# Performance work log

Hardware: AMD Instinct MI355X
Metric: run time of the kernel (lower is better)

The kernel has to match this reference:

```python
import jax, jax.numpy as jnp
import numpy as np

B, L, D = 16, 512, 768   # batch, seq_len, hidden_size
H = 12                   # encoder attention heads (self_attention_scores)
K = 128                  # num_preserved_tokens
U, NH = 256, 4           # router attention num_units / num_heads


def setup_inputs() -> dict:
    key = jax.random.key(0)
    ks = jax.random.split(key, 8)
    hidden_states = jax.random.normal(ks[0], (B, L, D), dtype=jnp.float32)
    u = jax.random.uniform(ks[1], (B, 1, 1, L))
    attention_mask = jnp.where(u < 0.9, 0.0, -10000.0).astype(jnp.float32)
    self_attention_scores = jax.random.normal(ks[2], (B, H, L, L), dtype=jnp.float32)
    Wq = jax.random.normal(ks[3], (U, D), dtype=jnp.float32) * 0.02
    Wk = jax.random.normal(ks[4], (U, D), dtype=jnp.float32) * 0.02
    Wv = jax.random.normal(ks[5], (U, D), dtype=jnp.float32) * 0.02
    Wo = jax.random.normal(ks[6], (D, U), dtype=jnp.float32) * 0.02
    bo = jnp.zeros((D,), dtype=jnp.float32)
    return {"hidden_states": hidden_states, "attention_mask": attention_mask,
            "self_attention_scores": self_attention_scores,
            "Wq": Wq, "Wk": Wk, "Wv": Wv, "Wo": Wo, "bo": bo}


def reference(hidden_states, attention_mask, self_attention_scores, Wq, Wk, Wv, Wo, bo):
    # sentence summary: softmax over additive mask -> weighted token average
    att = jax.nn.softmax(attention_mask, axis=-1)            # [B,1,1,L]
    sentences = jnp.einsum('bql,bld->bqd', att[:, 0], hidden_states)  # [B,1,D]

    key_padding_mask = attention_mask[:, 0, 0, :] < -10.0    # [B,L] True = masked

    # MyMultiHeadAttention(query=sentences, key=value=hidden_states)
    hd = U // NH
    q = jnp.einsum('bqd,ud->bqu', sentences, Wq)             # [B,1,U]
    k = jnp.einsum('bld,ud->blu', hidden_states, Wk)         # [B,L,U]
    v = jnp.einsum('bld,ud->blu', hidden_states, Wv)         # [B,L,U]
    qh = q.reshape(B, 1, NH, hd).transpose(2, 0, 1, 3)       # [h,B,1,hd]
    kh = k.reshape(B, L, NH, hd).transpose(2, 0, 1, 3)       # [h,B,L,hd]
    vh = v.reshape(B, L, NH, hd).transpose(2, 0, 1, 3)       # [h,B,L,hd]
    # NOTE: original scales by key_dim**0.5 = hidden_size**0.5 (not head dim)
    scores = jnp.einsum('hbqd,hbkd->hbqk', qh, kh) / (D ** 0.5)  # [h,B,1,L]
    scores = jnp.where(key_padding_mask[None, :, None, :], -jnp.inf, scores)
    probs = jax.nn.softmax(scores, axis=-1)
    out_h = jnp.einsum('hbqk,hbkd->hbqd', probs, vh)         # [h,B,1,hd]
    out = out_h.transpose(1, 2, 0, 3).reshape(B, 1, U)       # concat heads
    new_token = jnp.einsum('bqu,du->bqd', out, Wo) + bo      # [B,1,D]

    class_token = hidden_states[:, :1, :]                    # [B,1,D]

    # importance: mean over heads, sum over query positions -> [B,L]
    importance = self_attention_scores.mean(axis=1).sum(axis=1)
    top_idx = jax.lax.top_k(importance, K)[1]                # [B,K]
    # boolean-mask gather preserves original token order -> sort indices
    sorted_idx = jnp.sort(top_idx, axis=-1)                  # [B,K]
    preserved_tokens = jnp.take_along_axis(hidden_states, sorted_idx[:, :, None], axis=1)  # [B,K,D]
    preserved_mask = jnp.take_along_axis(attention_mask[:, 0, 0, :], sorted_idx, axis=1)
    preserved_mask = preserved_mask.reshape(B, 1, 1, K)

    zmask = jnp.zeros((B, 1, 1, 1), dtype=attention_mask.dtype)
    final_token = jnp.concatenate([class_token, preserved_tokens, new_token], axis=1)  # [B,K+2,D]
    final_attention_mask = jnp.concatenate([zmask, preserved_mask, zmask], axis=-1)    # [B,1,1,K+2]
    return final_token, final_attention_mask
```

## Files before the change

### kernel.cpp

```cpp
#include <hip/hip_runtime.h>
#include <math.h>

#define B_ 16
#define L_ 512
#define D_ 768
#define H_ 12
#define K_ 128
#define U_ 256
#define NH_ 4
#define HD_ 64
#define OUTROWS_ 130
#define IMPCH_ 64

__global__ __launch_bounds__(768) void front_kernel(
    const float* __restrict__ sas, const float* __restrict__ hidden,
    const float* __restrict__ mask, float* __restrict__ part,
    float* __restrict__ sent_part) {
  const int t = threadIdx.x;
  if (blockIdx.x < B_ * IMPCH_) {
    __shared__ float4 lbuf[6][128];
    const int b = blockIdx.x >> 6, chunk = blockIdx.x & 63;
    const int col4 = t & 127;
    const int rg = t >> 7;
    const float4* base = (const float4*)sas +
        ((size_t)(b * (H_ * L_) + chunk * 96 + rg * 16)) * 128 + col4;
    float4 a = make_float4(0.f, 0.f, 0.f, 0.f);
    #pragma unroll
    for (int k = 0; k < 16; ++k) {
      float4 v = base[(size_t)k * 128];
      a.x += v.x; a.y += v.y; a.z += v.z; a.w += v.w;
    }
    lbuf[rg][col4] = a;
    __syncthreads();
    if (rg == 0) {
      float4 o = lbuf[0][col4];
      #pragma unroll
      for (int g = 1; g < 6; ++g) {
        float4 v = lbuf[g][col4];
        o.x += v.x; o.y += v.y; o.z += v.z; o.w += v.w;
      }
      const float s = 1.0f / 12.0f;
      o.x *= s; o.y *= s; o.z *= s; o.w *= s;
      ((float4*)part)[((size_t)b * IMPCH_ + chunk) * 128 + col4] = o;
    }
  } else {
    __shared__ float att[L_];
    __shared__ float red_m[12], red_s[12];
    __shared__ float4 cbuf[4][192];
    const int i = blockIdx.x - B_ * IMPCH_;
    const int b = i >> 4, chunk = i & 15;
    const int wave = t >> 6, lane = t & 63;
    const float m = (t < L_) ? mask[b * L_ + t] : -INFINITY;
    float r = m;
    #pragma unroll
    for (int off = 32; off > 0; off >>= 1) r = fmaxf(r, __shfl_down(r, off, 64));
    if (lane == 0) red_m[wave] = r;
    __syncthreads();
    float mx = red_m[0];
    #pragma unroll
    for (int w = 1; w < 12; ++w) mx = fmaxf(mx, red_m[w]);
    const float e = (t < L_) ? expf(m - mx) : 0.f;
    float rs = e;
    #pragma unroll
    for (int off = 32; off > 0; off >>= 1) rs += __shfl_down(rs, off, 64);
    if (lane == 0) red_s[wave] = rs;
    __syncthreads();
    float se = 0.f;
    #pragma unroll
    for (int w = 0; w < 12; ++w) se += red_s[w];
    if (t < L_) att[t] = e / se;
    __syncthreads();
    const int c4 = t % 192, sub = t / 192;
    const int l0 = chunk * 32 + sub * 8;
    const float4* h4 = (const float4*)hidden + ((size_t)b * L_ + l0) * 192 + c4;
    float4 acc = make_float4(0.f, 0.f, 0.f, 0.f);
    #pragma unroll
    for (int ii = 0; ii < 8; ++ii) {
      const float w = att[l0 + ii];
      const float4 hv = h4[(size_t)ii * 192];
      acc.x += w * hv.x; acc.y += w * hv.y; acc.z += w * hv.z; acc.w += w * hv.w;
    }
    cbuf[sub][c4] = acc;
    __syncthreads();
    if (t < 192) {
      float4 o = cbuf[0][t];
      #pragma unroll
      for (int g = 1; g < 4; ++g) {
        const float4 v = cbuf[g][t];
        o.x += v.x; o.y += v.y; o.z += v.z; o.w += v.w;
      }
      ((float4*)sent_part)[((size_t)b * 16 + chunk) * 192 + t] = o;
    }
  }
}

__global__ __launch_bounds__(768) void qproj_topk_kernel(
    const float* __restrict__ sent_part, const float* __restrict__ Wq,
    const float* __restrict__ Wk, float* __restrict__ wqe,
    const float* __restrict__ part, const float* __restrict__ mask,
    const float* __restrict__ hidden, float* __restrict__ out0,
    float* __restrict__ out1, float* __restrict__ outv) {
  __shared__ float s[D_];
  __shared__ float qvh[HD_];
  __shared__ float v[L_];
  __shared__ int lidx[K_];
  __shared__ int wcnt[12];
  const int t = threadIdx.x;
  const int wave = t >> 6, lane = t & 63;

  if (blockIdx.x < 64) {
    const int b = blockIdx.x >> 2, h = blockIdx.x & 3;
    {
      const float* sp = sent_part + (size_t)b * 16 * D_ + t;
      float a = 0.f;
      #pragma unroll
      for (int c = 0; c < 16; ++c) a += sp[(size_t)c * D_];
      s[t] = a;
    }
    __syncthreads();
    for (int u = wave; u < HD_; u += 12) {
      const float* wr = Wq + (size_t)(h * HD_ + u) * D_;
      float acc = 0.f;
      #pragma unroll
      for (int k = 0; k < 12; ++k) {
        const int d = lane + (k << 6);
        acc += wr[d] * s[d];
      }
      #pragma unroll
      for (int o = 32; o > 0; o >>= 1) acc += __shfl_down(acc, o, 64);
      if (lane == 0) qvh[u] = acc;
    }
    __syncthreads();
    {
      float acc = 0.f;
      const float* wk = Wk + (size_t)(h * HD_) * D_ + t;
      #pragma unroll 4
      for (int j = 0; j < HD_; ++j) acc += qvh[j] * wk[(size_t)j * D_];
      wqe[((size_t)b * NH_ + h) * D_ + t] = acc;
    }
  } else {
    const int b = blockIdx.x - 64;
    if (t < U_) outv[b * U_ + t] = 0.f;
    if (t < L_) {
      const float* pp = part + (size_t)b * IMPCH_ * L_ + t;
      float sum = 0.f;
      #pragma unroll 8
      for (int g = 0; g < IMPCH_; ++g) sum += pp[(size_t)g * L_];
      v[t] = sum;
    }
    __syncthreads();
    bool sel = false;
    if (t < L_) {
      const float mv = v[t];
      int cnt = 0;
      #pragma unroll 8
      for (int j = 0; j < L_; ++j) {
        float o = v[j];
        cnt += (o > mv) || (o == mv && j < t);
      }
      sel = cnt < K_;
    }
    const unsigned long long ball = __ballot(sel);
    if (lane == 0) wcnt[wave] = __popcll(ball);
    __syncthreads();
    int base = 0;
    for (int w = 0; w < wave; ++w) base += wcnt[w];
    const int pos = base + __popcll(ball & ((1ull << lane) - 1ull));
    if (sel) {
      lidx[pos] = t;
      out1[b * OUTROWS_ + 1 + pos] = mask[b * L_ + t];
    }
    if (t == 0) {
      out1[b * OUTROWS_ + 0] = 0.f;
      out1[b * OUTROWS_ + OUTROWS_ - 1] = 0.f;
    }
    __syncthreads();
    const float4* hb4 = (const float4*)(hidden + (size_t)b * L_ * D_);
    float4* ob4 = (float4*)(out0 + (size_t)b * OUTROWS_ * D_);
    const int NG = (K_ + 1) * 192;
    for (int i = t; i < NG; i += 768) {
      const int r = i / 192;
      const int c = i - r * 192;
      const int src = (r == 0) ? 0 : lidx[r - 1];
      ob4[r * 192 + c] = hb4[src * 192 + c];
    }
  }
}

__global__ __launch_bounds__(256) void score_kernel(
    const float* __restrict__ hidden, const float* __restrict__ mask,
    const float* __restrict__ wqe, float* __restrict__ scores) {
  __shared__ float4 wq4[NH_ * 192];
  const int b = blockIdx.x, chunk = blockIdx.y, t = threadIdx.x;
  {
    const float4* wsrc = (const float4*)(wqe + (size_t)b * NH_ * D_);
    for (int i = t; i < NH_ * 192; i += 256) wq4[i] = wsrc[i];
  }
  __syncthreads();
  const int wave = t >> 6, lane = t & 63;
  const float scale = 0.03608439182435161f;
  #pragma unroll
  for (int r = 0; r < 8; ++r) {
    const int l = chunk * 32 + wave * 8 + r;
    const float4* hr4 = (const float4*)(hidden + ((size_t)b * L_ + l) * D_);
    float s0 = 0.f, s1 = 0.f, s2 = 0.f, s3 = 0.f;
    #pragma unroll
    for (int jj = 0; jj < 3; ++jj) {
      const int c = lane + 64 * jj;
      const float4 hv = hr4[c];
      const float4 w0 = wq4[0 * 192 + c];
      const float4 w1 = wq4[1 * 192 + c];
      const float4 w2 = wq4[2 * 192 + c];
      const float4 w3 = wq4[3 * 192 + c];
      s0 += hv.x * w0.x + hv.y * w0.y + hv.z * w0.z + hv.w * w0.w;
      s1 += hv.x * w1.x + hv.y * w1.y + hv.z * w1.z + hv.w * w1.w;
      s2 += hv.x * w2.x + hv.y * w2.y + hv.z * w2.z + hv.w * w2.w;
      s3 += hv.x * w3.x + hv.y * w3.y + hv.z * w3.z + hv.w * w3.w;
    }
    #pragma unroll
    for (int o = 32; o > 0; o >>= 1) {
      s0 += __shfl_down(s0, o, 64);
      s1 += __shfl_down(s1, o, 64);
      s2 += __shfl_down(s2, o, 64);
      s3 += __shfl_down(s3, o, 64);
    }
    if (lane == 0) {
      const bool kp = mask[b * L_ + l] < -10.f;
      float* sp = scores + (size_t)b * NH_ * L_ + l;
      sp[0 * L_] = kp ? -INFINITY : s0 * scale;
      sp[1 * L_] = kp ? -INFINITY : s1 * scale;
      sp[2 * L_] = kp ? -INFINITY : s2 * scale;
      sp[3 * L_] = kp ? -INFINITY : s3 * scale;
    }
  }
}

__global__ __launch_bounds__(768) void ctx_outv_kernel(
    const float* __restrict__ hidden, const float* __restrict__ scores,
    const float* __restrict__ Wv, float* __restrict__ outv) {
  __shared__ float pr[NH_][32];
  __shared__ float red_m[NH_][12], red_s[NH_][12];
  __shared__ __align__(16) float ctxs[NH_ * D_];
  const int b = blockIdx.x, chunk = blockIdx.y, t = threadIdx.x;
  const int wave = t >> 6, lane = t & 63;
  const int l0 = chunk * 32;

  float val[NH_];
  #pragma unroll
  for (int h = 0; h < NH_; ++h)
    val[h] = (t < L_) ? scores[((size_t)b * NH_ + h) * L_ + t] : -INFINITY;
  #pragma unroll
  for (int h = 0; h < NH_; ++h) {
    float r = val[h];
    #pragma unroll
    for (int off = 32; off > 0; off >>= 1) r = fmaxf(r, __shfl_down(r, off, 64));
    if (lane == 0) red_m[h][wave] = r;
  }
  __syncthreads();
  float e[NH_];
  #pragma unroll
  for (int h = 0; h < NH_; ++h) {
    float mx = red_m[h][0];
    #pragma unroll
    for (int w = 1; w < 12; ++w) mx = fmaxf(mx, red_m[h][w]);
    e[h] = (t < L_) ? expf(val[h] - mx) : 0.f;
    float rs = e[h];
    #pragma unroll
    for (int off = 32; off > 0; off >>= 1) rs += __shfl_down(rs, off, 64);
    if (lane == 0) red_s[h][wave] = rs;
  }
  __syncthreads();
  if (t >= l0 && t < l0 + 32) {
    #pragma unroll
    for (int h = 0; h < NH_; ++h) {
      float se = 0.f;
      #pragma unroll
      for (int w = 0; w < 12; ++w) se += red_s[h][w];
      pr[h][t - l0] = e[h] / se;
    }
  }
  __syncthreads();

  const int c4 = t % 192, hh = t / 192;
  const float4* h4 = (const float4*)hidden + ((size_t)b * L_ + l0) * 192 + c4;
  float4 acc = make_float4(0.f, 0.f, 0.f, 0.f);
  #pragma unroll 8
  for (int l = 0; l < 32; ++l) {
    const float w = pr[hh][l];
    const float4 hv = h4[(size_t)l * 192];
    acc.x += w * hv.x; acc.y += w * hv.y; acc.z += w * hv.z; acc.w += w * hv.w;
  }
  ((float4*)ctxs)[hh * 192 + c4] = acc;
  __syncthreads();

  for (int hu = wave; hu < U_; hu += 12) {
    const float* wr = Wv + (size_t)hu * D_;
    const float* ch = ctxs + (hu >> 6) * D_;
    float a = 0.f;
    #pragma unroll
    for (int k = 0; k < 12; ++k) {
      const int d = lane + (k << 6);
      a += wr[d] * ch[d];
    }
    #pragma unroll
    for (int off = 32; off > 0; off >>= 1) a += __shfl_down(a, off, 64);
    if (lane == 0) atomicAdd(&outv[b * U_ + hu], a);
  }
}

__global__ __launch_bounds__(192) void newtoken_kernel(
    const float* __restrict__ outv, const float* __restrict__ Wo,
    const float* __restrict__ bo, float* __restrict__ out0) {
  __shared__ float4 ov4[64];
  const int b = blockIdx.x, q = blockIdx.y, t = threadIdx.x;
  const int wave = t >> 6, lane = t & 63;
  if (t < 64) ov4[t] = ((const float4*)(outv + b * U_))[t];
  __syncthreads();
  const int dbase = q * 192 + wave * 64;
  const float4 o = ov4[lane];
  for (int i = 0; i < 64; ++i) {
    const int d = dbase + i;
    const float4 w = ((const float4*)(Wo + (size_t)d * U_))[lane];
    float acc = w.x * o.x + w.y * o.y + w.z * o.z + w.w * o.w;
    #pragma unroll
    for (int off = 32; off > 0; off >>= 1) acc += __shfl_down(acc, off, 64);
    if (lane == 0)
      out0[((size_t)b * OUTROWS_ + (OUTROWS_ - 1)) * D_ + d] = bo[d] + acc;
  }
}

extern "C" void kernel_launch(void* const* d_in, const int* in_sizes, int n_in,
                              void* d_out, int out_size, void* d_ws, size_t ws_size,
                              hipStream_t stream) {
  const float* hidden = (const float*)d_in[0];
  const float* mask   = (const float*)d_in[1];
  const float* sas    = (const float*)d_in[2];
  const float* Wq     = (const float*)d_in[3];
  const float* Wk     = (const float*)d_in[4];
  const float* Wv     = (const float*)d_in[5];
  const float* Wo     = (const float*)d_in[6];
  const float* bo     = (const float*)d_in[7];

  float* out0 = (float*)d_out;
  float* out1 = out0 + (size_t)B_ * OUTROWS_ * D_;

  float* part      = (float*)d_ws;
  float* sent_part = part + (size_t)B_ * IMPCH_ * L_;
  float* wqe       = sent_part + (size_t)B_ * 16 * D_;
  float* scores    = wqe + (size_t)B_ * NH_ * D_;
  float* outv      = scores + (size_t)B_ * NH_ * L_;

  front_kernel<<<B_ * IMPCH_ + B_ * 16, 768, 0, stream>>>(sas, hidden, mask,
                                                          part, sent_part);
  qproj_topk_kernel<<<80, 768, 0, stream>>>(sent_part, Wq, Wk, wqe,
                                            part, mask, hidden, out0, out1, outv);
  score_kernel<<<dim3(B_, 16), 256, 0, stream>>>(hidden, mask, wqe, scores);
  ctx_outv_kernel<<<dim3(B_, 16), 768, 0, stream>>>(hidden, scores, Wv, outv);
  newtoken_kernel<<<dim3(B_, 4), 192, 0, stream>>>(outv, Wo, bo, out0);
}
```

Measured before the change: 413.2 us.

## Fuse five kernels into two using atomic counters and in-kernel grid barriers

Merges the top-k/gather and query projection stages into the front kernel with last-block-done atomic counters. It also fuses the score, context and new-token stages into one kernel that uses per-batch spin barriers on a counter. The aim is to remove launch gaps and serialization between small kernels. It adds a memset, atomic spin-waits that rely on all 256 blocks being co-resident, and a serial tail done by the last block per batch.

```diff
diff --git a/kernel.cpp b/kernel.cpp
--- a/kernel.cpp
+++ b/kernel.cpp
@@ -12,13 +12,22 @@
 #define OUTROWS_ 130
 #define IMPCH_ 64
 
-__global__ __launch_bounds__(768) void front_kernel(
+__global__ __launch_bounds__(768) void front2_kernel(
     const float* __restrict__ sas, const float* __restrict__ hidden,
-    const float* __restrict__ mask, float* __restrict__ part,
-    float* __restrict__ sent_part) {
+    const float* __restrict__ mask, const float* __restrict__ Wq,
+    const float* __restrict__ Wk, float* __restrict__ part,
+    float* __restrict__ sent_part, float* __restrict__ wqe,
+    float* __restrict__ out0, float* __restrict__ out1,
+    unsigned int* __restrict__ cntT, unsigned int* __restrict__ cntQ) {
   const int t = threadIdx.x;
+  const int wave = t >> 6, lane = t & 63;
+
   if (blockIdx.x < B_ * IMPCH_) {
     __shared__ float4 lbuf[6][128];
+    __shared__ float v[L_];
+    __shared__ int lidx[K_];
+    __shared__ int wcnt[12];
+    __shared__ unsigned int lastT;
     const int b = blockIdx.x >> 6, chunk = blockIdx.x & 63;
     const int col4 = t & 127;
     const int rg = t >> 7;
@@ -27,8 +36,8 @@
     float4 a = make_float4(0.f, 0.f, 0.f, 0.f);
     #pragma unroll
     for (int k = 0; k < 16; ++k) {
-      float4 v = base[(size_t)k * 128];
-      a.x += v.x; a.y += v.y; a.z += v.z; a.w += v.w;
+      float4 vv = base[(size_t)k * 128];
+      a.x += vv.x; a.y += vv.y; a.z += vv.z; a.w += vv.w;
     }
     lbuf[rg][col4] = a;
     __syncthreads();
@@ -36,111 +45,22 @@
       float4 o = lbuf[0][col4];
       #pragma unroll
       for (int g = 1; g < 6; ++g) {
-        float4 v = lbuf[g][col4];
-        o.x += v.x; o.y += v.y; o.z += v.z; o.w += v.w;
+        float4 vv = lbuf[g][col4];
+        o.x += vv.x; o.y += vv.y; o.z += vv.z; o.w += vv.w;
       }
       const float s = 1.0f / 12.0f;
       o.x *= s; o.y *= s; o.z *= s; o.w *= s;
       ((float4*)part)[((size_t)b * IMPCH_ + chunk) * 128 + col4] = o;
     }
-  } else {
-    __shared__ float att[L_];
-    __shared__ float red_m[12], red_s[12];
-    __shared__ float4 cbuf[4][192];
-    const int i = blockIdx.x - B_ * IMPCH_;
-    const int b = i >> 4, chunk = i & 15;
-    const int wave = t >> 6, lane = t & 63;
-    const float m = (t < L_) ? mask[b * L_ + t] : -INFINITY;
-    float r = m;
-    #pragma unroll
-    for (int off = 32; off > 0; off >>= 1) r = fmaxf(r, __shfl_down(r, off, 64));
-    if (lane == 0) red_m[wave] = r;
-    __syncthreads();
-    float mx = red_m[0];
-    #pragma unroll
-    for (int w = 1; w < 12; ++w) mx = fmaxf(mx, red_m[w]);
-    const float e = (t < L_) ? expf(m - mx) : 0.f;
-    float rs = e;
-    #pragma unroll
-    for (int off = 32; off > 0; off >>= 1) rs += __shfl_down(rs, off, 64);
-    if (lane == 0) red_s[wave] = rs;
-    __syncthreads();
-    float se = 0.f;
-    #pragma unroll
-    for (int w = 0; w < 12; ++w) se += red_s[w];
-    if (t < L_) att[t] = e / se;
-    __syncthreads();
-    const int c4 = t % 192, sub = t / 192;
-    const int l0 = chunk * 32 + sub * 8;
-    const float4* h4 = (const float4*)hidden + ((size_t)b * L_ + l0) * 192 + c4;
-    float4 acc = make_float4(0.f, 0.f, 0.f, 0.f);
-    #pragma unroll
-    for (int ii = 0; ii < 8; ++ii) {
-      const float w = att[l0 + ii];
-      const float4 hv = h4[(size_t)ii * 192];
-      acc.x += w * hv.x; acc.y += w * hv.y; acc.z += w * hv.z; acc.w += w * hv.w;
-    }
-    cbuf[sub][c4] = acc;
-    __syncthreads();
-    if (t < 192) {
-      float4 o = cbuf[0][t];
-      #pragma unroll
-      for (int g = 1; g < 4; ++g) {
-        const float4 v = cbuf[g][t];
-        o.x += v.x; o.y += v.y; o.z += v.z; o.w += v.w;
-      }
-      ((float4*)sent_part)[((size_t)b * 16 + chunk) * 192 + t] = o;
-    }
-  }
-}
-
-__global__ __launch_bounds__(768) void qproj_topk_kernel(
-    const float* __restrict__ sent_part, const float* __restrict__ Wq,
-    const float* __restrict__ Wk, float* __restrict__ wqe,
-    const float* __restrict__ part, const float* __restrict__ mask,
-    const float* __restrict__ hidden, float* __restrict__ out0,
-    float* __restrict__ out1, float* __restrict__ outv) {
-  __shared__ float s[D_];
-  __shared__ float qvh[HD_];
-  __shared__ float v[L_];
-  __shared__ int lidx[K_];
-  __shared__ int wcnt[12];
-  const int t = threadIdx.x;
-  const int wave = t >> 6, lane = t & 63;
-
-  if (blockIdx.x < 64) {
-    const int b = blockIdx.x >> 2, h = blockIdx.x & 3;
-    {
-      const float* sp = sent_part + (size_t)b * 16 * D_ + t;
-      float a = 0.f;
-      #pragma unroll
-      for (int c = 0; c < 16; ++c) a += sp[(size_t)c * D_];
-      s[t] = a;
-    }
-    __syncthreads();
-    for (int u = wave; u < HD_; u += 12) {
-      const float* wr = Wq + (size_t)(h * HD_ + u) * D_;
-      float acc = 0.f;
-      #pragma unroll
-      for (int k = 0; k < 12; ++k) {
-        const int d = lane + (k << 6);
-        acc += wr[d] * s[d];
-      }
-      #pragma unroll
-      for (int o = 32; o > 0; o >>= 1) acc += __shfl_down(acc, o, 64);
-      if (lane == 0) qvh[u] = acc;
-    }
-    __syncthreads();
-    {
-      float acc = 0.f;
-      const float* wk = Wk + (size_t)(h * HD_) * D_ + t;
-      #pragma unroll 4
-      for (int j = 0; j < HD_; ++j) acc += qvh[j] * wk[(size_t)j * D_];
-      wqe[((size_t)b * NH_ + h) * D_ + t] = acc;
-    }
-  } else {
-    const int b = blockIdx.x - 64;
-    if (t < U_) outv[b * U_ + t] = 0.f;
+    __syncthreads();
+    if (t == 0) {
+      __threadfence();
+      lastT = (atomicAdd(&cntT[b], 1u) == IMPCH_ - 1) ? 1u : 0u;
+    }
+    __syncthreads();
+    if (!lastT) return;
+    __threadfence();
+
     if (t < L_) {
       const float* pp = part + (size_t)b * IMPCH_ * L_ + t;
       float sum = 0.f;
@@ -163,9 +83,9 @@
     const unsigned long long ball = __ballot(sel);
     if (lane == 0) wcnt[wave] = __popcll(ball);
     __syncthreads();
-    int base = 0;
-    for (int w = 0; w < wave; ++w) base += wcnt[w];
-    const int pos = base + __popcll(ball & ((1ull << lane) - 1ull));
+    int bsum = 0;
+    for (int w = 0; w < wave; ++w) bsum += wcnt[w];
+    const int pos = bsum + __popcll(ball & ((1ull << lane) - 1ull));
     if (sel) {
       lidx[pos] = t;
       out1[b * OUTROWS_ + 1 + pos] = mask[b * L_ + t];
@@ -184,66 +104,160 @@
       const int src = (r == 0) ? 0 : lidx[r - 1];
       ob4[r * 192 + c] = hb4[src * 192 + c];
     }
+  } else {
+    __shared__ float att[L_];
+    __shared__ float red_m[12], red_s[12];
+    __shared__ float4 cbuf[4][192];
+    __shared__ float s[D_];
+    __shared__ float qvh[U_];
+    __shared__ unsigned int lastQ;
+    const int i = blockIdx.x - B_ * IMPCH_;
+    const int b = i >> 4, chunk = i & 15;
+    const float m = (t < L_) ? mask[b * L_ + t] : -INFINITY;
+    float r = m;
+    #pragma unroll
+    for (int off = 32; off > 0; off >>= 1) r = fmaxf(r, __shfl_down(r, off, 64));
+    if (lane == 0) red_m[wave] = r;
+    __syncthreads();
+    float mx = red_m[0];
+    #pragma unroll
+    for (int w = 1; w < 12; ++w) mx = fmaxf(mx, red_m[w]);
+    const float e = (t < L_) ? expf(m - mx) : 0.f;
+    float rs = e;
+    #pragma unroll
+    for (int off = 32; off > 0; off >>= 1) rs += __shfl_down(rs, off, 64);
+    if (lane == 0) red_s[wave] = rs;
+    __syncthreads();
+    float se = 0.f;
+    #pragma unroll
+    for (int w = 0; w < 12; ++w) se += red_s[w];
+    if (t < L_) att[t] = e / se;
+    __syncthreads();
+    const int c4 = t % 192, sub = t / 192;
+    const int l0 = chunk * 32 + sub * 8;
+    const float4* h4 = (const float4*)hidden + ((size_t)b * L_ + l0) * 192 + c4;
+    float4 acc = make_float4(0.f, 0.f, 0.f, 0.f);
+    #pragma unroll
+    for (int ii = 0; ii < 8; ++ii) {
+      const float w = att[l0 + ii];
+      const float4 hv = h4[(size_t)ii * 192];
+      acc.x += w * hv.x; acc.y += w * hv.y; acc.z += w * hv.z; acc.w += w * hv.w;
+    }
+    cbuf[sub][c4] = acc;
+    __syncthreads();
+    if (t < 192) {
+      float4 o = cbuf[0][t];
+      #pragma unroll
+      for (int g = 1; g < 4; ++g) {
+        const float4 vv = cbuf[g][t];
+        o.x += vv.x; o.y += vv.y; o.z += vv.z; o.w += vv.w;
+      }
+      ((float4*)sent_part)[((size_t)b * 16 + chunk) * 192 + t] = o;
+    }
+    __syncthreads();
+    if (t == 0) {
+      __threadfence();
+      lastQ = (atomicAdd(&cntQ[b], 1u) == 15u) ? 1u : 0u;
+    }
+    __syncthreads();
+    if (!lastQ) return;
+    __threadfence();
+
+    {
+      const float* sp = sent_part + (size_t)b * 16 * D_ + t;
+      float aa = 0.f;
+      #pragma unroll
+      for (int c = 0; c < 16; ++c) aa += sp[(size_t)c * D_];
+      s[t] = aa;
+    }
+    __syncthreads();
+    for (int idx = wave; idx < U_; idx += 12) {
+      const float* wr = Wq + (size_t)idx * D_;
+      float acc2 = 0.f;
+      #pragma unroll
+      for (int k = 0; k < 12; ++k) {
+        const int d = lane + (k << 6);
+        acc2 += wr[d] * s[d];
+      }
+      #pragma unroll
+      for (int o = 32; o > 0; o >>= 1) acc2 += __shfl_down(acc2, o, 64);
+      if (lane == 0) qvh[idx] = acc2;
+    }
+    __syncthreads();
+    #pragma unroll
+    for (int h = 0; h < NH_; ++h) {
+      float acc2 = 0.f;
+      const float* wk = Wk + (size_t)(h * HD_) * D_ + t;
+      #pragma unroll 4
+      for (int j = 0; j < HD_; ++j) acc2 += qvh[h * HD_ + j] * wk[(size_t)j * D_];
+      wqe[((size_t)b * NH_ + h) * D_ + t] = acc2;
+    }
   }
 }
 
-__global__ __launch_bounds__(256) void score_kernel(
+__global__ __launch_bounds__(768) void attn_kernel(
     const float* __restrict__ hidden, const float* __restrict__ mask,
-    const float* __restrict__ wqe, float* __restrict__ scores) {
+    const float* __restrict__ wqe, const float* __restrict__ Wv,
+    const float* __restrict__ Wo, const float* __restrict__ bo,
+    float* __restrict__ scores, float* __restrict__ outv,
+    unsigned int* __restrict__ cntC, float* __restrict__ out0) {
   __shared__ float4 wq4[NH_ * 192];
-  const int b = blockIdx.x, chunk = blockIdx.y, t = threadIdx.x;
-  {
-    const float4* wsrc = (const float4*)(wqe + (size_t)b * NH_ * D_);
-    for (int i = t; i < NH_ * 192; i += 256) wq4[i] = wsrc[i];
-  }
-  __syncthreads();
-  const int wave = t >> 6, lane = t & 63;
-  const float scale = 0.03608439182435161f;
-  #pragma unroll
-  for (int r = 0; r < 8; ++r) {
-    const int l = chunk * 32 + wave * 8 + r;
-    const float4* hr4 = (const float4*)(hidden + ((size_t)b * L_ + l) * D_);
-    float s0 = 0.f, s1 = 0.f, s2 = 0.f, s3 = 0.f;
-    #pragma unroll
-    for (int jj = 0; jj < 3; ++jj) {
-      const int c = lane + 64 * jj;
-      const float4 hv = hr4[c];
-      const float4 w0 = wq4[0 * 192 + c];
-      const float4 w1 = wq4[1 * 192 + c];
-      const float4 w2 = wq4[2 * 192 + c];
-      const float4 w3 = wq4[3 * 192 + c];
-      s0 += hv.x * w0.x + hv.y * w0.y + hv.z * w0.z + hv.w * w0.w;
-      s1 += hv.x * w1.x + hv.y * w1.y + hv.z * w1.z + hv.w * w1.w;
-      s2 += hv.x * w2.x + hv.y * w2.y + hv.z * w2.z + hv.w * w2.w;
-      s3 += hv.x * w3.x + hv.y * w3.y + hv.z * w3.z + hv.w * w3.w;
-    }
-    #pragma unroll
-    for (int o = 32; o > 0; o >>= 1) {
-      s0 += __shfl_down(s0, o, 64);
-      s1 += __shfl_down(s1, o, 64);
-      s2 += __shfl_down(s2, o, 64);
-      s3 += __shfl_down(s3, o, 64);
-    }
-    if (lane == 0) {
-      const bool kp = mask[b * L_ + l] < -10.f;
-      float* sp = scores + (size_t)b * NH_ * L_ + l;
-      sp[0 * L_] = kp ? -INFINITY : s0 * scale;
-      sp[1 * L_] = kp ? -INFINITY : s1 * scale;
-      sp[2 * L_] = kp ? -INFINITY : s2 * scale;
-      sp[3 * L_] = kp ? -INFINITY : s3 * scale;
-    }
-  }
-}
-
-__global__ __launch_bounds__(768) void ctx_outv_kernel(
-    const float* __restrict__ hidden, const float* __restrict__ scores,
-    const float* __restrict__ Wv, float* __restrict__ outv) {
   __shared__ float pr[NH_][32];
   __shared__ float red_m[NH_][12], red_s[NH_][12];
   __shared__ __align__(16) float ctxs[NH_ * D_];
+  __shared__ float4 ov4[64];
   const int b = blockIdx.x, chunk = blockIdx.y, t = threadIdx.x;
   const int wave = t >> 6, lane = t & 63;
   const int l0 = chunk * 32;
+
+  for (int i = t; i < NH_ * 192; i += 768)
+    wq4[i] = ((const float4*)(wqe + (size_t)b * NH_ * D_))[i];
+  __syncthreads();
+  const float scale = 0.03608439182435161f;
+  if (wave < 8) {
+    #pragma unroll
+    for (int r = 0; r < 4; ++r) {
+      const int l = l0 + wave * 4 + r;
+      const float4* hr4 = (const float4*)(hidden + ((size_t)b * L_ + l) * D_);
+      float s0 = 0.f, s1 = 0.f, s2 = 0.f, s3 = 0.f;
+      #pragma unroll
+      for (int jj = 0; jj < 3; ++jj) {
+        const int c = lane + 64 * jj;
+        const float4 hv = hr4[c];
+        const float4 w0 = wq4[0 * 192 + c];
+        const float4 w1 = wq4[1 * 192 + c];
+        const float4 w2 = wq4[2 * 192 + c];
+        const float4 w3 = wq4[3 * 192 + c];
+        s0 += hv.x * w0.x + hv.y * w0.y + hv.z * w0.z + hv.w * w0.w;
+        s1 += hv.x * w1.x + hv.y * w1.y + hv.z * w1.z + hv.w * w1.w;
+        s2 += hv.x * w2.x + hv.y * w2.y + hv.z * w2.z + hv.w * w2.w;
+        s3 += hv.x * w3.x + hv.y * w3.y + hv.z * w3.z + hv.w * w3.w;
+      }
+      #pragma unroll
+      for (int o = 32; o > 0; o >>= 1) {
+        s0 += __shfl_down(s0, o, 64);
+        s1 += __shfl_down(s1, o, 64);
+        s2 += __shfl_down(s2, o, 64);
+        s3 += __shfl_down(s3, o, 64);
+      }
+      if (lane == 0) {
+        const bool kp = mask[b * L_ + l] < -10.f;
+        float* sp = scores + (size_t)b * NH_ * L_ + l;
+        sp[0 * L_] = kp ? -INFINITY : s0 * scale;
+        sp[1 * L_] = kp ? -INFINITY : s1 * scale;
+        sp[2 * L_] = kp ? -INFINITY : s2 * scale;
+        sp[3 * L_] = kp ? -INFINITY : s3 * scale;
+      }
+    }
+  }
+  __syncthreads();
+  if (t == 0) {
+    __threadfence();
+    atomicAdd(&cntC[b], 1u);
+    while (atomicAdd(&cntC[b], 0u) < 16u) __builtin_amdgcn_s_sleep(1);
+  }
+  __syncthreads();
+  __threadfence();
 
   float val[NH_];
   #pragma unroll
@@ -280,19 +294,19 @@
     }
   }
   __syncthreads();
-
-  const int c4 = t % 192, hh = t / 192;
-  const float4* h4 = (const float4*)hidden + ((size_t)b * L_ + l0) * 192 + c4;
-  float4 acc = make_float4(0.f, 0.f, 0.f, 0.f);
-  #pragma unroll 8
-  for (int l = 0; l < 32; ++l) {
-    const float w = pr[hh][l];
-    const float4 hv = h4[(size_t)l * 192];
-    acc.x += w * hv.x; acc.y += w * hv.y; acc.z += w * hv.z; acc.w += w * hv.w;
-  }
-  ((float4*)ctxs)[hh * 192 + c4] = acc;
-  __syncthreads();
-
+  {
+    const int c4 = t % 192, hh = t / 192;
+    const float4* h4 = (const float4*)hidden + ((size_t)b * L_ + l0) * 192 + c4;
+    float4 acc = make_float4(0.f, 0.f, 0.f, 0.f);
+    #pragma unroll 8
+    for (int l = 0; l < 32; ++l) {
+      const float w = pr[hh][l];
+      const float4 hv = h4[(size_t)l * 192];
+      acc.x += w * hv.x; acc.y += w * hv.y; acc.z += w * hv.z; acc.w += w * hv.w;
+    }
+    ((float4*)ctxs)[hh * 192 + c4] = acc;
+  }
+  __syncthreads();
   for (int hu = wave; hu < U_; hu += 12) {
     const float* wr = Wv + (size_t)hu * D_;
     const float* ch = ctxs + (hu >> 6) * D_;
@@ -306,20 +320,28 @@
     for (int off = 32; off > 0; off >>= 1) a += __shfl_down(a, off, 64);
     if (lane == 0) atomicAdd(&outv[b * U_ + hu], a);
   }
-}
-
-__global__ __launch_bounds__(192) void newtoken_kernel(
-    const float* __restrict__ outv, const float* __restrict__ Wo,
-    const float* __restrict__ bo, float* __restrict__ out0) {
-  __shared__ float4 ov4[64];
-  const int b = blockIdx.x, q = blockIdx.y, t = threadIdx.x;
-  const int wave = t >> 6, lane = t & 63;
-  if (t < 64) ov4[t] = ((const float4*)(outv + b * U_))[t];
-  __syncthreads();
-  const int dbase = q * 192 + wave * 64;
+  __syncthreads();
+  if (t == 0) {
+    __threadfence();
+    atomicAdd(&cntC[b], 1u);
+    while (atomicAdd(&cntC[b], 0u) < 32u) __builtin_amdgcn_s_sleep(1);
+  }
+  __syncthreads();
+
+  if (t < 64) {
+    float* op = outv + (size_t)b * U_ + t * 4;
+    float4 vv;
+    vv.x = atomicAdd(op + 0, 0.f);
+    vv.y = atomicAdd(op + 1, 0.f);
+    vv.z = atomicAdd(op + 2, 0.f);
+    vv.w = atomicAdd(op + 3, 0.f);
+    ov4[t] = vv;
+  }
+  __syncthreads();
   const float4 o = ov4[lane];
-  for (int i = 0; i < 64; ++i) {
-    const int d = dbase + i;
+  #pragma unroll
+  for (int i = 0; i < 4; ++i) {
+    const int d = chunk * 48 + wave * 4 + i;
     const float4 w = ((const float4*)(Wo + (size_t)d * U_))[lane];
     float acc = w.x * o.x + w.y * o.y + w.z * o.z + w.w * o.w;
     #pragma unroll
@@ -344,17 +366,18 @@
   float* out0 = (float*)d_out;
   float* out1 = out0 + (size_t)B_ * OUTROWS_ * D_;
 
-  float* part      = (float*)d_ws;
+  unsigned int* cntT = (unsigned int*)d_ws;
+  unsigned int* cntQ = cntT + 16;
+  unsigned int* cntC = cntQ + 16;
+  float* outv      = (float*)d_ws + 64;
+  float* part      = outv + (size_t)B_ * U_;
   float* sent_part = part + (size_t)B_ * IMPCH_ * L_;
   float* wqe       = sent_part + (size_t)B_ * 16 * D_;
   float* scores    = wqe + (size_t)B_ * NH_ * D_;
-  float* outv      = scores + (size_t)B_ * NH_ * L_;
-
-  front_kernel<<<B_ * IMPCH_ + B_ * 16, 768, 0, stream>>>(sas, hidden, mask,
-                                                          part, sent_part);
-  qproj_topk_kernel<<<80, 768, 0, stream>>>(sent_part, Wq, Wk, wqe,
-                                            part, mask, hidden, out0, out1, outv);
-  score_kernel<<<dim3(B_, 16), 256, 0, stream>>>(hidden, mask, wqe, scores);
-  ctx_outv_kernel<<<dim3(B_, 16), 768, 0, stream>>>(hidden, scores, Wv, outv);
-  newtoken_kernel<<<dim3(B_, 4), 192, 0, stream>>>(outv, Wo, bo, out0);
+
+  hipMemsetAsync(d_ws, 0, (64 + (size_t)B_ * U_) * sizeof(float), stream);
+  front2_kernel<<<B_ * IMPCH_ + B_ * 16, 768, 0, stream>>>(
+      sas, hidden, mask, Wq, Wk, part, sent_part, wqe, out0, out1, cntT, cntQ);
+  attn_kernel<<<dim3(B_, 16), 768, 0, stream>>>(
+      hidden, mask, wqe, Wv, Wo, bo, scores, outv, cntC, out0);
 }
```

Result: slower. 651.3 us (+57.6%).

## Fuse context, Wv projection and output projection into one per-batch tail kernel

Applied to the files above, without the earlier changes.

Merges ctx_outv_kernel and newtoken_kernel into one kernel with a single block per batch. Each block now accumulates the full 512-token context, projects it through Wv into shared memory, then applies Wo and bias directly. This drops one launch, the atomics and the zeroing of the outv buffer. In exchange, parallelism falls from 256 blocks to 16, so each block streams all of its batch's hidden rows serially.

```diff
diff --git a/kernel.cpp b/kernel.cpp
--- a/kernel.cpp
+++ b/kernel.cpp
@@ -99,7 +99,7 @@
     const float* __restrict__ Wk, float* __restrict__ wqe,
     const float* __restrict__ part, const float* __restrict__ mask,
     const float* __restrict__ hidden, float* __restrict__ out0,
-    float* __restrict__ out1, float* __restrict__ outv) {
+    float* __restrict__ out1) {
   __shared__ float s[D_];
   __shared__ float qvh[HD_];
   __shared__ float v[L_];
@@ -140,7 +140,6 @@
     }
   } else {
     const int b = blockIdx.x - 64;
-    if (t < U_) outv[b * U_ + t] = 0.f;
     if (t < L_) {
       const float* pp = part + (size_t)b * IMPCH_ * L_ + t;
       float sum = 0.f;
@@ -235,15 +234,16 @@
   }
 }
 
-__global__ __launch_bounds__(768) void ctx_outv_kernel(
+__global__ __launch_bounds__(768) void tail_kernel(
     const float* __restrict__ hidden, const float* __restrict__ scores,
-    const float* __restrict__ Wv, float* __restrict__ outv) {
-  __shared__ float pr[NH_][32];
+    const float* __restrict__ Wv, const float* __restrict__ Wo,
+    const float* __restrict__ bo, float* __restrict__ out0) {
+  __shared__ float pr[NH_][L_];
   __shared__ float red_m[NH_][12], red_s[NH_][12];
   __shared__ __align__(16) float ctxs[NH_ * D_];
-  const int b = blockIdx.x, chunk = blockIdx.y, t = threadIdx.x;
+  __shared__ __align__(16) float ovs[U_];
+  const int b = blockIdx.x, t = threadIdx.x;
   const int wave = t >> 6, lane = t & 63;
-  const int l0 = chunk * 32;
 
   float val[NH_];
   #pragma unroll
@@ -270,27 +270,29 @@
     if (lane == 0) red_s[h][wave] = rs;
   }
   __syncthreads();
-  if (t >= l0 && t < l0 + 32) {
+  if (t < L_) {
     #pragma unroll
     for (int h = 0; h < NH_; ++h) {
       float se = 0.f;
       #pragma unroll
       for (int w = 0; w < 12; ++w) se += red_s[h][w];
-      pr[h][t - l0] = e[h] / se;
-    }
-  }
-  __syncthreads();
-
-  const int c4 = t % 192, hh = t / 192;
-  const float4* h4 = (const float4*)hidden + ((size_t)b * L_ + l0) * 192 + c4;
-  float4 acc = make_float4(0.f, 0.f, 0.f, 0.f);
-  #pragma unroll 8
-  for (int l = 0; l < 32; ++l) {
-    const float w = pr[hh][l];
-    const float4 hv = h4[(size_t)l * 192];
-    acc.x += w * hv.x; acc.y += w * hv.y; acc.z += w * hv.z; acc.w += w * hv.w;
-  }
-  ((float4*)ctxs)[hh * 192 + c4] = acc;
+      pr[h][t] = e[h] / se;
+    }
+  }
+  __syncthreads();
+
+  {
+    const int c4 = t % 192, hh = t / 192;
+    const float4* h4 = (const float4*)hidden + (size_t)b * L_ * 192 + c4;
+    float4 acc = make_float4(0.f, 0.f, 0.f, 0.f);
+    #pragma unroll 4
+    for (int l = 0; l < L_; ++l) {
+      const float w = pr[hh][l];
+      const float4 hv = h4[(size_t)l * 192];
+      acc.x += w * hv.x; acc.y += w * hv.y; acc.z += w * hv.z; acc.w += w * hv.w;
+    }
+    ((float4*)ctxs)[hh * 192 + c4] = acc;
+  }
   __syncthreads();
 
   for (int hu = wave; hu < U_; hu += 12) {
@@ -304,22 +306,12 @@
     }
     #pragma unroll
     for (int off = 32; off > 0; off >>= 1) a += __shfl_down(a, off, 64);
-    if (lane == 0) atomicAdd(&outv[b * U_ + hu], a);
-  }
-}
-
-__global__ __launch_bounds__(192) void newtoken_kernel(
-    const float* __restrict__ outv, const float* __restrict__ Wo,
-    const float* __restrict__ bo, float* __restrict__ out0) {
-  __shared__ float4 ov4[64];
-  const int b = blockIdx.x, q = blockIdx.y, t = threadIdx.x;
-  const int wave = t >> 6, lane = t & 63;
-  if (t < 64) ov4[t] = ((const float4*)(outv + b * U_))[t];
-  __syncthreads();
-  const int dbase = q * 192 + wave * 64;
-  const float4 o = ov4[lane];
-  for (int i = 0; i < 64; ++i) {
-    const int d = dbase + i;
+    if (lane == 0) ovs[hu] = a;
+  }
+  __syncthreads();
+
+  const float4 o = ((const float4*)ovs)[lane];
+  for (int d = wave; d < D_; d += 12) {
     const float4 w = ((const float4*)(Wo + (size_t)d * U_))[lane];
     float acc = w.x * o.x + w.y * o.y + w.z * o.z + w.w * o.w;
     #pragma unroll
@@ -348,13 +340,11 @@
   float* sent_part = part + (size_t)B_ * IMPCH_ * L_;
   float* wqe       = sent_part + (size_t)B_ * 16 * D_;
   float* scores    = wqe + (size_t)B_ * NH_ * D_;
-  float* outv      = scores + (size_t)B_ * NH_ * L_;
 
   front_kernel<<<B_ * IMPCH_ + B_ * 16, 768, 0, stream>>>(sas, hidden, mask,
                                                           part, sent_part);
   qproj_topk_kernel<<<80, 768, 0, stream>>>(sent_part, Wq, Wk, wqe,
-                                            part, mask, hidden, out0, out1, outv);
+                                            part, mask, hidden, out0, out1);
   score_kernel<<<dim3(B_, 16), 256, 0, stream>>>(hidden, mask, wqe, scores);
-  ctx_outv_kernel<<<dim3(B_, 16), 768, 0, stream>>>(hidden, scores, Wv, outv);
-  newtoken_kernel<<<dim3(B_, 4), 192, 0, stream>>>(outv, Wo, bo, out0);
-}
+  tail_kernel<<<B_, 768, 0, stream>>>(hidden, scores, Wv, Wo, bo, out0);
+}
```

New measurement: 459.1 us. +11.1%, slower.
